# Optimization experiments

Measured on AMD Instinct MI355X. Metric: run time of the kernel, lower is better.

Reference implementation:

```python
import jax, jax.numpy as jnp
import numpy as np


def setup_inputs() -> dict:
    key = jax.random.key(0)
    k1, k2 = jax.random.split(key)
    pred = jax.random.normal(k1, (4, 8192, 3), dtype=jnp.float32)
    gt = jax.random.normal(k2, (4, 8192, 3), dtype=jnp.float32)
    return {"pred": pred, "gt": gt}


def reference(pred, gt):
    # pairwise squared distances: [B, N, M]
    diff = pred[:, :, None, :] - gt[:, None, :, :]
    distances = jnp.sum(diff ** 2, axis=-1)
    pred_to_gt = jnp.min(distances, axis=2)  # [B, N]
    gt_to_pred = jnp.min(distances, axis=1)  # [B, M]
    return jnp.mean(pred_to_gt) + jnp.mean(gt_to_pred)
```

## Files before the change

### kernel.cpp

```cpp
#include <hip/hip_runtime.h>
#include <math.h>


typedef _Float16 half8 __attribute__((ext_vector_type(8)));
typedef float f32x16 __attribute__((ext_vector_type(16)));

#define NPTS   8192
#define CLOUD  32768
#define NQ_TOT 65536
#define TT     512
#define NTC    16

__device__ __forceinline__ void split2(float v, _Float16& h, _Float16& l) {
  h = (_Float16)v; l = (_Float16)(v - (float)h);
}

__device__ __forceinline__ float min_fold(float m, const f32x16& d) {
  float a = fminf(fminf(d[0], d[1]), d[2]);
  float b = fminf(fminf(d[3], d[4]), d[5]);
  float c = fminf(fminf(d[6], d[7]), d[8]);
  float e = fminf(fminf(d[9], d[10]), d[11]);
  float f = fminf(fminf(d[12], d[13]), d[14]);
  float g = fminf(fminf(a, b), c);
  float h = fminf(fminf(e, f), d[15]);
  return fminf(m, fminf(g, h));
}

__global__ __launch_bounds__(256, 6) void chamfer_mfma(
    const float* __restrict__ pred, const float* __restrict__ gt,
    unsigned int* __restrict__ minbits, float* __restrict__ out) {
  __shared__ __align__(16) half8 lds[TT * 2];
  int bid = blockIdx.x;
  int tc   = bid & (NTC - 1);
  int qblk = (bid >> 4) & 31;
  int b    = (bid >> 9) & 3;
  int dir  = bid >> 11;
  const float* qsrc = dir ? gt : pred;
  const float* tsrc = dir ? pred : gt;
  int t = threadIdx.x, lane = t & 63, wave = t >> 6;
  if (bid == 0 && t == 0) out[0] = 0.f;

  const float* qb = qsrc + (size_t)(b * NPTS + qblk * 256 + wave * 64) * 3;
  int qi0 = (lane & 31), qi1 = (lane & 31) + 32;
  float q0x = qb[3 * qi0], q0y = qb[3 * qi0 + 1], q0z = qb[3 * qi0 + 2];
  float q1x = qb[3 * qi1], q1y = qb[3 * qi1 + 1], q1z = qb[3 * qi1 + 2];

  const float* tb = tsrc + (size_t)(b * NPTS + tc * TT) * 3;
  for (int k = t; k < TT; k += 256) {
    float x = tb[3 * k], y = tb[3 * k + 1], z = tb[3 * k + 2];
    float s = x * x + y * y + z * z;
    _Float16 xh, xl, yh, yl, zh, zl, sh, sl;
    split2(x, xh, xl); split2(y, yh, yl); split2(z, zh, zl); split2(s, sh, sl);
    _Float16 Xh = (_Float16)(-2.f * (float)xh), Xl = (_Float16)(-2.f * (float)xl);
    _Float16 Yh = (_Float16)(-2.f * (float)yh), Yl = (_Float16)(-2.f * (float)yl);
    _Float16 Zh = (_Float16)(-2.f * (float)zh), Zl = (_Float16)(-2.f * (float)zl);
    _Float16 one = (_Float16)1.0f;
    lds[2 * k]     = (half8){Xh, Xl, Xh, Xl, Yh, Yl, Yh, Yl};
    lds[2 * k + 1] = (half8){Zh, Zl, Zh, Zl, sh, sl, one, one};
  }

  half8 bq0, bq1;
  {
    float s0 = q0x * q0x + q0y * q0y + q0z * q0z;
    float s1 = q1x * q1x + q1y * q1y + q1z * q1z;
    _Float16 x0h, x0l, y0h, y0l, z0h, z0l, s0h, s0l;
    _Float16 x1h, x1l, y1h, y1l, z1h, z1l, s1h, s1l;
    split2(q0x, x0h, x0l); split2(q0y, y0h, y0l); split2(q0z, z0h, z0l); split2(s0, s0h, s0l);
    split2(q1x, x1h, x1l); split2(q1y, y1h, y1l); split2(q1z, z1h, z1l); split2(s1, s1h, s1l);
    _Float16 one = (_Float16)1.0f;
    bq0 = (lane < 32) ? (half8){x0h, x0h, x0l, x0l, y0h, y0h, y0l, y0l}
                      : (half8){z0h, z0h, z0l, z0l, one, one, s0h, s0l};
    bq1 = (lane < 32) ? (half8){x1h, x1h, x1l, x1l, y1h, y1h, y1l, y1l}
                      : (half8){z1h, z1h, z1l, z1l, one, one, s1h, s1l};
  }
  __syncthreads();

  int arow = 2 * (lane & 31) + (lane >> 5);
  float m0 = INFINITY, m1 = INFINITY;
  f32x16 zero = {};
  #pragma unroll 2
  for (int g = 0; g < TT / 32; ++g) {
    half8 a = lds[arow + g * 64];
    f32x16 d0 = __builtin_amdgcn_mfma_f32_32x32x16_f16(a, bq0, zero, 0, 0, 0);
    f32x16 d1 = __builtin_amdgcn_mfma_f32_32x32x16_f16(a, bq1, zero, 0, 0, 0);
    m0 = min_fold(m0, d0);
    m1 = min_fold(m1, d1);
  }
  m0 = fminf(m0, __shfl_xor(m0, 32, 64));
  m1 = fminf(m1, __shfl_xor(m1, 32, 64));

  if (lane < 32) {
    size_t qi = (size_t)dir * CLOUD + b * NPTS + qblk * 256 + wave * 64 + (lane & 31);
    atomicMin(&minbits[qi],      __float_as_uint(fmaxf(m0, 0.f)));
    atomicMin(&minbits[qi + 32], __float_as_uint(fmaxf(m1, 0.f)));
  }
}

__global__ __launch_bounds__(256) void reduce_kernel(
    const unsigned int* __restrict__ minbits, float* __restrict__ out) {
  __shared__ float wsum[4];
  float acc = 0.f;
  for (int i = blockIdx.x * 256 + threadIdx.x; i < NQ_TOT; i += 64 * 256)
    acc += __uint_as_float(minbits[i]);
  acc *= (1.0f / 32768.0f);
  #pragma unroll
  for (int off = 32; off > 0; off >>= 1) acc += __shfl_down(acc, off, 64);
  int wid = threadIdx.x >> 6;
  if ((threadIdx.x & 63) == 0) wsum[wid] = acc;
  __syncthreads();
  if (threadIdx.x == 0) atomicAdd(out, wsum[0] + wsum[1] + wsum[2] + wsum[3]);
}

extern "C" void kernel_launch(void* const* d_in, const int* in_sizes, int n_in,
                              void* d_out, int out_size, void* d_ws, size_t ws_size,
                              hipStream_t stream) {
  const float* pred = (const float*)d_in[0];
  const float* gt   = (const float*)d_in[1];
  float* out = (float*)d_out;
  unsigned int* minbits = (unsigned int*)d_ws;

  chamfer_mfma<<<4096, 256, 0, stream>>>(pred, gt, minbits, out);
  reduce_kernel<<<64, 256, 0, stream>>>(minbits, out);
}
```

Measured before the change: 76.38 us.

## Prepack fp16-split points in a pre-pass and load tiles via global_load_lds

Adds a pack_points kernel that converts every point once into the split fp16 A/B operand layouts and stores them in workspace. The main kernel then copies target tiles straight into LDS with global_load_lds and reads query operands directly, so each of the 4096 blocks no longer repeats the split/convert work. This costs one extra kernel launch and extra workspace traffic. The min_fold reduction tree is also reassociated.

```diff
diff --git a/kernel.cpp b/kernel.cpp
--- a/kernel.cpp
+++ b/kernel.cpp
@@ -11,76 +11,85 @@
 #define TT     512
 #define NTC    16
 
+#define PT_OFF (256 * 1024)
+#define PQ_OFF (256 * 1024 + 2 * 1024 * 1024)
+
+typedef __attribute__((address_space(1))) const unsigned int as1_uint;
+typedef __attribute__((address_space(3))) unsigned int as3_uint;
+
 __device__ __forceinline__ void split2(float v, _Float16& h, _Float16& l) {
   h = (_Float16)v; l = (_Float16)(v - (float)h);
 }
 
 __device__ __forceinline__ float min_fold(float m, const f32x16& d) {
-  float a = fminf(fminf(d[0], d[1]), d[2]);
-  float b = fminf(fminf(d[3], d[4]), d[5]);
-  float c = fminf(fminf(d[6], d[7]), d[8]);
-  float e = fminf(fminf(d[9], d[10]), d[11]);
-  float f = fminf(fminf(d[12], d[13]), d[14]);
-  float g = fminf(fminf(a, b), c);
-  float h = fminf(fminf(e, f), d[15]);
-  return fminf(m, fminf(g, h));
+  float t0 = fminf(fminf(d[0], d[1]), d[2]);
+  float t1 = fminf(fminf(d[3], d[4]), d[5]);
+  float t2 = fminf(fminf(d[6], d[7]), d[8]);
+  float t3 = fminf(fminf(d[9], d[10]), d[11]);
+  float t4 = fminf(fminf(d[12], d[13]), d[14]);
+  float t5 = fminf(fminf(t0, t1), d[15]);
+  float t6 = fminf(fminf(t2, t3), t4);
+  return fminf(m, fminf(t5, t6));
+}
+
+__global__ __launch_bounds__(256) void pack_points(
+    const float* __restrict__ pred, const float* __restrict__ gt,
+    half8* __restrict__ pt, half8* __restrict__ pq, float* __restrict__ out) {
+  int id = blockIdx.x * 256 + threadIdx.x;
+  if (id == 0) out[0] = 0.f;
+  int cloud = id >> 15;
+  int idx = id & (CLOUD - 1);
+  const float* src = cloud ? gt : pred;
+  float x = src[3 * idx], y = src[3 * idx + 1], z = src[3 * idx + 2];
+  float s = x * x + y * y + z * z;
+  _Float16 xh, xl, yh, yl, zh, zl, sh, sl;
+  split2(x, xh, xl); split2(y, yh, yl); split2(z, zh, zl); split2(s, sh, sl);
+  _Float16 one = (_Float16)1.0f;
+
+  size_t qbase = (size_t)cloud * 65536 + (size_t)idx * 2;
+  pq[qbase]     = (half8){xh, xh, xl, xl, yh, yh, yl, yl};
+  pq[qbase + 1] = (half8){zh, zh, zl, zl, one, one, sh, sl};
+
+  _Float16 Xh = (_Float16)(-2.f * (float)xh), Xl = (_Float16)(-2.f * (float)xl);
+  _Float16 Yh = (_Float16)(-2.f * (float)yh), Yl = (_Float16)(-2.f * (float)yl);
+  _Float16 Zh = (_Float16)(-2.f * (float)zh), Zl = (_Float16)(-2.f * (float)zl);
+  size_t tbase = (size_t)(cloud ^ 1) * 65536 + (size_t)(idx >> 5) * 64 + (idx & 31);
+  pt[tbase]      = (half8){Xh, Xl, Xh, Xl, Yh, Yl, Yh, Yl};
+  pt[tbase + 32] = (half8){Zh, Zl, Zh, Zl, sh, sl, one, one};
 }
 
 __global__ __launch_bounds__(256, 6) void chamfer_mfma(
-    const float* __restrict__ pred, const float* __restrict__ gt,
-    unsigned int* __restrict__ minbits, float* __restrict__ out) {
+    const half8* __restrict__ pt, const half8* __restrict__ pq,
+    unsigned int* __restrict__ minbits) {
   __shared__ __align__(16) half8 lds[TT * 2];
   int bid = blockIdx.x;
   int tc   = bid & (NTC - 1);
   int qblk = (bid >> 4) & 31;
   int b    = (bid >> 9) & 3;
   int dir  = bid >> 11;
-  const float* qsrc = dir ? gt : pred;
-  const float* tsrc = dir ? pred : gt;
   int t = threadIdx.x, lane = t & 63, wave = t >> 6;
-  if (bid == 0 && t == 0) out[0] = 0.f;
 
-  const float* qb = qsrc + (size_t)(b * NPTS + qblk * 256 + wave * 64) * 3;
-  int qi0 = (lane & 31), qi1 = (lane & 31) + 32;
-  float q0x = qb[3 * qi0], q0y = qb[3 * qi0 + 1], q0z = qb[3 * qi0 + 2];
-  float q1x = qb[3 * qi1], q1y = qb[3 * qi1 + 1], q1z = qb[3 * qi1 + 2];
-
-  const float* tb = tsrc + (size_t)(b * NPTS + tc * TT) * 3;
-  for (int k = t; k < TT; k += 256) {
-    float x = tb[3 * k], y = tb[3 * k + 1], z = tb[3 * k + 2];
-    float s = x * x + y * y + z * z;
-    _Float16 xh, xl, yh, yl, zh, zl, sh, sl;
-    split2(x, xh, xl); split2(y, yh, yl); split2(z, zh, zl); split2(s, sh, sl);
-    _Float16 Xh = (_Float16)(-2.f * (float)xh), Xl = (_Float16)(-2.f * (float)xl);
-    _Float16 Yh = (_Float16)(-2.f * (float)yh), Yl = (_Float16)(-2.f * (float)yl);
-    _Float16 Zh = (_Float16)(-2.f * (float)zh), Zl = (_Float16)(-2.f * (float)zl);
-    _Float16 one = (_Float16)1.0f;
-    lds[2 * k]     = (half8){Xh, Xl, Xh, Xl, Yh, Yl, Yh, Yl};
-    lds[2 * k + 1] = (half8){Zh, Zl, Zh, Zl, sh, sl, one, one};
+  const half8* gsrc = pt + (size_t)dir * 65536 + (size_t)b * 16384 + (size_t)tc * 1024;
+  #pragma unroll
+  for (int i = 0; i < 4; ++i) {
+    int seg = i * 4 + wave;
+    __builtin_amdgcn_global_load_lds((as1_uint*)(gsrc + seg * 64 + lane),
+                                     (as3_uint*)&lds[seg * 64], 16, 0, 0);
   }
 
-  half8 bq0, bq1;
-  {
-    float s0 = q0x * q0x + q0y * q0y + q0z * q0z;
-    float s1 = q1x * q1x + q1y * q1y + q1z * q1z;
-    _Float16 x0h, x0l, y0h, y0l, z0h, z0l, s0h, s0l;
-    _Float16 x1h, x1l, y1h, y1l, z1h, z1l, s1h, s1l;
-    split2(q0x, x0h, x0l); split2(q0y, y0h, y0l); split2(q0z, z0h, z0l); split2(s0, s0h, s0l);
-    split2(q1x, x1h, x1l); split2(q1y, y1h, y1l); split2(q1z, z1h, z1l); split2(s1, s1h, s1l);
-    _Float16 one = (_Float16)1.0f;
-    bq0 = (lane < 32) ? (half8){x0h, x0h, x0l, x0l, y0h, y0h, y0l, y0l}
-                      : (half8){z0h, z0h, z0l, z0l, one, one, s0h, s0l};
-    bq1 = (lane < 32) ? (half8){x1h, x1h, x1l, x1l, y1h, y1h, y1l, y1l}
-                      : (half8){z1h, z1h, z1l, z1l, one, one, s1h, s1l};
-  }
+  int hi = lane >> 5, ql = lane & 31;
+  int qstart = qblk * 256 + wave * 64;
+  const half8* pqb = pq + (size_t)dir * 65536 + (size_t)b * 16384 + (size_t)qstart * 2;
+  half8 bq0 = pqb[2 * ql + hi];
+  half8 bq1 = pqb[2 * (ql + 32) + hi];
+
   __syncthreads();
 
-  int arow = 2 * (lane & 31) + (lane >> 5);
   float m0 = INFINITY, m1 = INFINITY;
   f32x16 zero = {};
   #pragma unroll 2
   for (int g = 0; g < TT / 32; ++g) {
-    half8 a = lds[arow + g * 64];
+    half8 a = lds[g * 64 + lane];
     f32x16 d0 = __builtin_amdgcn_mfma_f32_32x32x16_f16(a, bq0, zero, 0, 0, 0);
     f32x16 d1 = __builtin_amdgcn_mfma_f32_32x32x16_f16(a, bq1, zero, 0, 0, 0);
     m0 = min_fold(m0, d0);
@@ -90,7 +99,7 @@
   m1 = fminf(m1, __shfl_xor(m1, 32, 64));
 
   if (lane < 32) {
-    size_t qi = (size_t)dir * CLOUD + b * NPTS + qblk * 256 + wave * 64 + (lane & 31);
+    size_t qi = (size_t)dir * CLOUD + (size_t)b * NPTS + qstart + ql;
     atomicMin(&minbits[qi],      __float_as_uint(fmaxf(m0, 0.f)));
     atomicMin(&minbits[qi + 32], __float_as_uint(fmaxf(m1, 0.f)));
   }
@@ -118,7 +127,10 @@
   const float* gt   = (const float*)d_in[1];
   float* out = (float*)d_out;
   unsigned int* minbits = (unsigned int*)d_ws;
+  half8* pt = (half8*)((char*)d_ws + PT_OFF);
+  half8* pq = (half8*)((char*)d_ws + PQ_OFF);
 
-  chamfer_mfma<<<4096, 256, 0, stream>>>(pred, gt, minbits, out);
+  pack_points<<<256, 256, 0, stream>>>(pred, gt, pt, pq, out);
+  chamfer_mfma<<<4096, 256, 0, stream>>>(pt, pq, minbits);
   reduce_kernel<<<64, 256, 0, stream>>>(minbits, out);
 }
```

After: 78.40 us. 1.03x slower.

## Loop each block over all target chunks, removing atomicMin and split-K grid

Applied to the files above, without the earlier changes.

Each block now handles 256 queries against the whole target cloud, looping over 16 chunks in LDS and prefetching the next chunk's points into registers while the current chunk is processed. This removes the global atomicMin scratch array and gives a deterministic per-block partial sum reduced by a single-block final kernel. The cost is a grid of only 256 blocks with one block per SM in the launch bounds, which lowers occupancy and may underfill the GPU. The chunk loop also adds barriers on every iteration.

```diff
diff --git a/kernel.cpp b/kernel.cpp
--- a/kernel.cpp
+++ b/kernel.cpp
@@ -6,59 +6,53 @@
 typedef float f32x16 __attribute__((ext_vector_type(16)));
 
 #define NPTS   8192
-#define CLOUD  32768
-#define NQ_TOT 65536
 #define TT     512
-#define NTC    16
+#define NCH    16
 
 __device__ __forceinline__ void split2(float v, _Float16& h, _Float16& l) {
   h = (_Float16)v; l = (_Float16)(v - (float)h);
 }
 
 __device__ __forceinline__ float min_fold(float m, const f32x16& d) {
-  float a = fminf(fminf(d[0], d[1]), d[2]);
-  float b = fminf(fminf(d[3], d[4]), d[5]);
-  float c = fminf(fminf(d[6], d[7]), d[8]);
-  float e = fminf(fminf(d[9], d[10]), d[11]);
-  float f = fminf(fminf(d[12], d[13]), d[14]);
-  float g = fminf(fminf(a, b), c);
-  float h = fminf(fminf(e, f), d[15]);
-  return fminf(m, fminf(g, h));
+  float t0 = fminf(fminf(d[0], d[1]), d[2]);
+  float t1 = fminf(fminf(d[3], d[4]), d[5]);
+  float t2 = fminf(fminf(d[6], d[7]), d[8]);
+  float t3 = fminf(fminf(d[9], d[10]), d[11]);
+  float t4 = fminf(fminf(d[12], d[13]), d[14]);
+  float t5 = fminf(fminf(t0, t1), d[15]);
+  float t6 = fminf(fminf(t2, t3), t4);
+  return fminf(m, fminf(t5, t6));
 }
 
-__global__ __launch_bounds__(256, 6) void chamfer_mfma(
+__device__ __forceinline__ void pack_target(float x, float y, float z,
+                                            half8& fa, half8& fb) {
+  float s = x * x + y * y + z * z;
+  _Float16 xh, xl, yh, yl, zh, zl, sh, sl;
+  split2(x, xh, xl); split2(y, yh, yl); split2(z, zh, zl); split2(s, sh, sl);
+  _Float16 one = (_Float16)1.0f;
+  _Float16 Xh = (_Float16)(-2.f * (float)xh), Xl = (_Float16)(-2.f * (float)xl);
+  _Float16 Yh = (_Float16)(-2.f * (float)yh), Yl = (_Float16)(-2.f * (float)yl);
+  _Float16 Zh = (_Float16)(-2.f * (float)zh), Zl = (_Float16)(-2.f * (float)zl);
+  fa = (half8){Xh, Xl, Xh, Xl, Yh, Yl, Yh, Yl};
+  fb = (half8){Zh, Zl, Zh, Zl, sh, sl, one, one};
+}
+
+__global__ __launch_bounds__(256, 1) void chamfer_full(
     const float* __restrict__ pred, const float* __restrict__ gt,
-    unsigned int* __restrict__ minbits, float* __restrict__ out) {
+    float* __restrict__ partial) {
   __shared__ __align__(16) half8 lds[TT * 2];
+  __shared__ float wsum[4];
   int bid = blockIdx.x;
-  int tc   = bid & (NTC - 1);
-  int qblk = (bid >> 4) & 31;
-  int b    = (bid >> 9) & 3;
-  int dir  = bid >> 11;
+  int qblk = bid & 31;
+  int b    = (bid >> 5) & 3;
+  int dir  = bid >> 7;
   const float* qsrc = dir ? gt : pred;
   const float* tsrc = dir ? pred : gt;
-  int t = threadIdx.x, lane = t & 63, wave = t >> 6;
-  if (bid == 0 && t == 0) out[0] = 0.f;
+  int t = threadIdx.x, lane = t & 63, wave = t >> 6, ql = lane & 31;
 
   const float* qb = qsrc + (size_t)(b * NPTS + qblk * 256 + wave * 64) * 3;
-  int qi0 = (lane & 31), qi1 = (lane & 31) + 32;
-  float q0x = qb[3 * qi0], q0y = qb[3 * qi0 + 1], q0z = qb[3 * qi0 + 2];
-  float q1x = qb[3 * qi1], q1y = qb[3 * qi1 + 1], q1z = qb[3 * qi1 + 2];
-
-  const float* tb = tsrc + (size_t)(b * NPTS + tc * TT) * 3;
-  for (int k = t; k < TT; k += 256) {
-    float x = tb[3 * k], y = tb[3 * k + 1], z = tb[3 * k + 2];
-    float s = x * x + y * y + z * z;
-    _Float16 xh, xl, yh, yl, zh, zl, sh, sl;
-    split2(x, xh, xl); split2(y, yh, yl); split2(z, zh, zl); split2(s, sh, sl);
-    _Float16 Xh = (_Float16)(-2.f * (float)xh), Xl = (_Float16)(-2.f * (float)xl);
-    _Float16 Yh = (_Float16)(-2.f * (float)yh), Yl = (_Float16)(-2.f * (float)yl);
-    _Float16 Zh = (_Float16)(-2.f * (float)zh), Zl = (_Float16)(-2.f * (float)zl);
-    _Float16 one = (_Float16)1.0f;
-    lds[2 * k]     = (half8){Xh, Xl, Xh, Xl, Yh, Yl, Yh, Yl};
-    lds[2 * k + 1] = (half8){Zh, Zl, Zh, Zl, sh, sl, one, one};
-  }
-
+  float q0x = qb[3 * ql],        q0y = qb[3 * ql + 1],        q0z = qb[3 * ql + 2];
+  float q1x = qb[3 * (ql + 32)], q1y = qb[3 * (ql + 32) + 1], q1z = qb[3 * (ql + 32) + 2];
   half8 bq0, bq1;
   {
     float s0 = q0x * q0x + q0y * q0y + q0z * q0z;
@@ -73,42 +67,66 @@
     bq1 = (lane < 32) ? (half8){x1h, x1h, x1l, x1l, y1h, y1h, y1l, y1l}
                       : (half8){z1h, z1h, z1l, z1l, one, one, s1h, s1l};
   }
-  __syncthreads();
 
-  int arow = 2 * (lane & 31) + (lane >> 5);
+  const float* tb = tsrc + (size_t)b * NPTS * 3;
+  float p0x, p0y, p0z, p1x, p1y, p1z;
+  {
+    const float* s0 = tb + (size_t)t * 3;
+    const float* s1 = tb + (size_t)(t + 256) * 3;
+    p0x = s0[0]; p0y = s0[1]; p0z = s0[2];
+    p1x = s1[0]; p1y = s1[1]; p1z = s1[2];
+  }
+
   float m0 = INFINITY, m1 = INFINITY;
   f32x16 zero = {};
-  #pragma unroll 2
-  for (int g = 0; g < TT / 32; ++g) {
-    half8 a = lds[arow + g * 64];
-    f32x16 d0 = __builtin_amdgcn_mfma_f32_32x32x16_f16(a, bq0, zero, 0, 0, 0);
-    f32x16 d1 = __builtin_amdgcn_mfma_f32_32x32x16_f16(a, bq1, zero, 0, 0, 0);
-    m0 = min_fold(m0, d0);
-    m1 = min_fold(m1, d1);
+  for (int tc = 0; tc < NCH; ++tc) {
+    half8 f0a, f0b, f1a, f1b;
+    pack_target(p0x, p0y, p0z, f0a, f0b);
+    pack_target(p1x, p1y, p1z, f1a, f1b);
+    if (tc) __syncthreads();
+    int base0 = (t >> 5) * 64 + (t & 31);
+    lds[base0]            = f0a;
+    lds[base0 + 32]       = f0b;
+    lds[base0 + 512]      = f1a;
+    lds[base0 + 512 + 32] = f1b;
+    if (tc + 1 < NCH) {
+      const float* s0 = tb + (size_t)((tc + 1) * TT + t) * 3;
+      const float* s1 = tb + (size_t)((tc + 1) * TT + t + 256) * 3;
+      p0x = s0[0]; p0y = s0[1]; p0z = s0[2];
+      p1x = s1[0]; p1y = s1[1]; p1z = s1[2];
+    }
+    __syncthreads();
+    #pragma unroll 2
+    for (int g = 0; g < TT / 32; ++g) {
+      half8 a = lds[g * 64 + lane];
+      f32x16 d0 = __builtin_amdgcn_mfma_f32_32x32x16_f16(a, bq0, zero, 0, 0, 0);
+      f32x16 d1 = __builtin_amdgcn_mfma_f32_32x32x16_f16(a, bq1, zero, 0, 0, 0);
+      m0 = min_fold(m0, d0);
+      m1 = min_fold(m1, d1);
+    }
   }
   m0 = fminf(m0, __shfl_xor(m0, 32, 64));
   m1 = fminf(m1, __shfl_xor(m1, 32, 64));
 
-  if (lane < 32) {
-    size_t qi = (size_t)dir * CLOUD + b * NPTS + qblk * 256 + wave * 64 + (lane & 31);
-    atomicMin(&minbits[qi],      __float_as_uint(fmaxf(m0, 0.f)));
-    atomicMin(&minbits[qi + 32], __float_as_uint(fmaxf(m1, 0.f)));
-  }
+  float v = (lane < 32) ? (fmaxf(m0, 0.f) + fmaxf(m1, 0.f)) : 0.f;
+  #pragma unroll
+  for (int off = 32; off > 0; off >>= 1) v += __shfl_down(v, off, 64);
+  if (lane == 0) wsum[wave] = v;
+  __syncthreads();
+  if (t == 0) partial[bid] = wsum[0] + wsum[1] + wsum[2] + wsum[3];
 }
 
-__global__ __launch_bounds__(256) void reduce_kernel(
-    const unsigned int* __restrict__ minbits, float* __restrict__ out) {
+__global__ __launch_bounds__(256) void final_reduce(
+    const float* __restrict__ partial, float* __restrict__ out) {
   __shared__ float wsum[4];
-  float acc = 0.f;
-  for (int i = blockIdx.x * 256 + threadIdx.x; i < NQ_TOT; i += 64 * 256)
-    acc += __uint_as_float(minbits[i]);
-  acc *= (1.0f / 32768.0f);
+  float v = partial[threadIdx.x];
   #pragma unroll
-  for (int off = 32; off > 0; off >>= 1) acc += __shfl_down(acc, off, 64);
-  int wid = threadIdx.x >> 6;
-  if ((threadIdx.x & 63) == 0) wsum[wid] = acc;
+  for (int off = 32; off > 0; off >>= 1) v += __shfl_down(v, off, 64);
+  int wave = threadIdx.x >> 6;
+  if ((threadIdx.x & 63) == 0) wsum[wave] = v;
   __syncthreads();
-  if (threadIdx.x == 0) atomicAdd(out, wsum[0] + wsum[1] + wsum[2] + wsum[3]);
+  if (threadIdx.x == 0)
+    out[0] = (wsum[0] + wsum[1] + wsum[2] + wsum[3]) * (1.0f / 32768.0f);
 }
 
 extern "C" void kernel_launch(void* const* d_in, const int* in_sizes, int n_in,
@@ -117,8 +135,8 @@
   const float* pred = (const float*)d_in[0];
   const float* gt   = (const float*)d_in[1];
   float* out = (float*)d_out;
-  unsigned int* minbits = (unsigned int*)d_ws;
+  float* partial = (float*)d_ws;
 
-  chamfer_mfma<<<4096, 256, 0, stream>>>(pred, gt, minbits, out);
-  reduce_kernel<<<64, 256, 0, stream>>>(minbits, out);
+  chamfer_full<<<256, 256, 0, stream>>>(pred, gt, partial);
+  final_reduce<<<1, 256, 0, stream>>>(partial, out);
 }
```

After: 105.7 us. 1.38x slower.
